# Performance work log

Hardware: AMD Instinct MI355X
Metric: run time of the kernel (lower is better)

Reference implementation:

```python
import jax, jax.numpy as jnp
import numpy as np

B, T, U, D = 2, 512, 48, 512
H, K = 1024, 128  # hidden_channels, num_classes; fc1 in = 2*D = 1024


def setup_inputs() -> dict:
    key = jax.random.key(0)
    ks = jax.random.split(key, 9)
    s = 0.02
    return {
        "img_feature": jax.random.normal(ks[0], (B, T, D), jnp.float32),
        "label_feature": jax.random.normal(ks[1], (B, U, D), jnp.float32),
        "masks": jnp.ones((B, 1, T), jnp.float32),
        "W1": jax.random.normal(ks[2], (H, 2 * D), jnp.float32) * s,
        "b1": jnp.zeros((H,), jnp.float32),
        "W2": jax.random.normal(ks[3], (K, H), jnp.float32) * s,
        "b2": jnp.zeros((K,), jnp.float32),
        "conv_w": jax.random.normal(ks[4], (K, D), jnp.float32) * s,
        "conv_b": jnp.zeros((K,), jnp.float32),
    }


def reference(img_feature, label_feature, masks, W1, b1, W2, b2, conv_w, conv_b):
    # pointwise Conv1d over img features: (B,T,D) -> (B,K,T), masked
    img_seg_score = (jnp.einsum('btd,kd->bkt', img_feature, conv_w)
                     + conv_b[None, :, None]) * masks
    # fc1(cat(label, img)) == label @ Wl^T + img @ Wi^T + b1 (broadcast add),
    # avoiding the O(B*U*T*2D) repeat+cat intermediate.
    d = label_feature.shape[-1]
    Wl, Wi = W1[:, :d], W1[:, d:]
    lab = jnp.einsum('bud,hd->buh', label_feature, Wl)  # (B,U,H)
    img = jnp.einsum('btd,hd->bth', img_feature, Wi)    # (B,T,H)
    h = jnp.tanh(lab[:, :, None, :] + img[:, None, :, :] + b1)  # (B,U,T,H)
    joint = jnp.einsum('buth,kh->butk', h, W2) + b2
    joint_score = jax.nn.log_softmax(joint, axis=-1)
    return (img_seg_score, joint_score)
```

## Files before the change

### kernel.cpp

```cpp
#include <hip/hip_runtime.h>
#include <math.h>

#define BB 2
#define TT 512
#define UU 48
#define DD 512
#define HH 1024
#define KK 128

typedef _Float16 f16x8 __attribute__((ext_vector_type(8)));
typedef __fp16 fp16x2_t __attribute__((ext_vector_type(2)));
typedef float floatx4 __attribute__((ext_vector_type(4)));

__device__ __forceinline__ f16x8 tanh8z(f16x8 z) {
    f16x8 o;
#pragma unroll
    for (int i = 0; i < 8; i += 2) {
        float e0 = __builtin_amdgcn_exp2f((float)z[i]);
        float e1 = __builtin_amdgcn_exp2f((float)z[i + 1]);
        float r0 = __builtin_amdgcn_rcpf(e0 + 1.0f);
        float r1 = __builtin_amdgcn_rcpf(e1 + 1.0f);
        fp16x2_t p = __builtin_amdgcn_cvt_pkrtz(fmaf(-2.0f, r0, 1.0f),
                                                fmaf(-2.0f, r1, 1.0f));
        o[i] = (_Float16)p[0];
        o[i + 1] = (_Float16)p[1];
    }
    return o;
}

__global__ __launch_bounds__(256) void mid_kernel5(
    const float* __restrict__ img, const float* __restrict__ labf,
    const float* __restrict__ W1, const float* __restrict__ W2,
    const float* __restrict__ conv_w,
    const float* __restrict__ b1, const float* __restrict__ conv_b,
    const float* __restrict__ masks,
    _Float16* __restrict__ imgHf, _Float16* __restrict__ labHf,
    _Float16* __restrict__ W2s, float* __restrict__ seg_out) {
    int bid = blockIdx.x, tid = threadIdx.x;
    if (bid >= 624) {
        int base = (bid - 624) * 256 + tid;
#pragma unroll
        for (int i = 0; i < 32; ++i) {
            int o = base + i * 4096;
            int hg = o >> 10, kk2 = (o >> 3) & 127, hl = o & 7;
            W2s[o] = (_Float16)W2[(size_t)kk2 * HH + hg * 8 + hl];
        }
        return;
    }
    __shared__ __align__(16) _Float16 a_s[32][72];
    __shared__ __align__(16) _Float16 w_s[4096];
    const float* Arow;
    const float* Wbase;
    int r0, n0b, wstride, region;
    if (bid < 512) {
        region = 0; Arow = img; Wbase = W1 + 512; wstride = 2 * DD;
        int xcd = bid & 7, j = bid >> 3;
        r0 = (j & 31) * 32; n0b = (xcd * 2 + (j >> 5)) * 64;
    } else if (bid < 560) {
        region = 1; Arow = labf; Wbase = W1; wstride = 2 * DD;
        int i = bid - 512; r0 = (i % 3) * 32; n0b = (i / 3) * 64;
    } else {
        region = 2; Arow = img; Wbase = conv_w; wstride = DD;
        int i = bid - 560; r0 = (i >> 1) * 32; n0b = (i & 1) * 64;
    }
    int lane = tid & 63, wv = tid >> 6;
    int m0 = (wv & 1) * 16, n0w = (wv >> 1) * 32;
    int q = lane >> 4, r = lane & 15;
    int arow = tid >> 3, acol = (tid & 7) * 8;
    int wn = tid >> 2, wk0 = (tid & 3) * 16;
    const float* aptr = &Arow[(size_t)(r0 + arow) * DD + acol];
    const float* wptr = &Wbase[(size_t)(n0b + wn) * wstride + wk0];
    floatx4 acc[2] = {};
    float4 pa0, pa1, pw[4];
    pa0 = *(const float4*)aptr;
    pa1 = *(const float4*)(aptr + 4);
#pragma unroll
    for (int i2 = 0; i2 < 4; ++i2) pw[i2] = *(const float4*)(wptr + i2 * 4);
    for (int c = 0; c < 8; ++c) {
        f16x8 av;
        av[0] = (_Float16)pa0.x; av[1] = (_Float16)pa0.y;
        av[2] = (_Float16)pa0.z; av[3] = (_Float16)pa0.w;
        av[4] = (_Float16)pa1.x; av[5] = (_Float16)pa1.y;
        av[6] = (_Float16)pa1.z; av[7] = (_Float16)pa1.w;
        *(f16x8*)&a_s[arow][acol] = av;
        f16x8 w0, w1;
        w0[0] = (_Float16)pw[0].x; w0[1] = (_Float16)pw[0].y;
        w0[2] = (_Float16)pw[0].z; w0[3] = (_Float16)pw[0].w;
        w0[4] = (_Float16)pw[1].x; w0[5] = (_Float16)pw[1].y;
        w0[6] = (_Float16)pw[1].z; w0[7] = (_Float16)pw[1].w;
        w1[0] = (_Float16)pw[2].x; w1[1] = (_Float16)pw[2].y;
        w1[2] = (_Float16)pw[2].z; w1[3] = (_Float16)pw[2].w;
        w1[4] = (_Float16)pw[3].x; w1[5] = (_Float16)pw[3].y;
        w1[6] = (_Float16)pw[3].z; w1[7] = (_Float16)pw[3].w;
        int kg = wk0 >> 3;
        *(f16x8*)&w_s[((kg + 0) * 64 + wn) * 8] = w0;
        *(f16x8*)&w_s[((kg + 1) * 64 + wn) * 8] = w1;
        __syncthreads();
        if (c < 7) {
            int cb = (c + 1) * 64;
            pa0 = *(const float4*)(aptr + cb);
            pa1 = *(const float4*)(aptr + cb + 4);
#pragma unroll
            for (int i2 = 0; i2 < 4; ++i2)
                pw[i2] = *(const float4*)(wptr + cb + i2 * 4);
        }
#pragma unroll
        for (int kt = 0; kt < 2; ++kt) {
            f16x8 af = *(const f16x8*)&a_s[m0 + r][kt * 32 + q * 8];
#pragma unroll
            for (int nt = 0; nt < 2; ++nt) {
                f16x8 bf = *(const f16x8*)
                    &w_s[((kt * 4 + q) * 64 + n0w + nt * 16 + r) * 8];
                acc[nt] = __builtin_amdgcn_mfma_f32_16x16x32_f16(
                    af, bf, acc[nt], 0, 0, 0);
            }
        }
        __syncthreads();
    }
    const float SC = 2.8853900817779268f;
    if (region == 0) {
#pragma unroll
        for (int nt = 0; nt < 2; ++nt) {
            int n = n0b + n0w + nt * 16 + r;
#pragma unroll
            for (int rr = 0; rr < 4; ++rr)
                imgHf[(size_t)(r0 + m0 + 4 * q + rr) * HH + n] =
                    (_Float16)(acc[nt][rr] * SC);
        }
    } else if (region == 1) {
#pragma unroll
        for (int nt = 0; nt < 2; ++nt) {
            int n = n0b + n0w + nt * 16 + r;
            float bv = b1[n];
#pragma unroll
            for (int rr = 0; rr < 4; ++rr)
                labHf[(size_t)(r0 + m0 + 4 * q + rr) * HH + n] =
                    (_Float16)((acc[nt][rr] + bv) * SC);
        }
    } else {
#pragma unroll
        for (int nt = 0; nt < 2; ++nt) {
            int k = n0b + n0w + nt * 16 + r;
            float bv = conv_b[k];
#pragma unroll
            for (int rr = 0; rr < 4; ++rr) {
                int row = r0 + m0 + 4 * q + rr;
                int b = row >> 9, t = row & 511;
                seg_out[((size_t)b * KK + k) * TT + t] =
                    (acc[nt][rr] + bv) * masks[row];
            }
        }
    }
}

__global__ __launch_bounds__(192, 2) void joint_kernel7(
    const _Float16* __restrict__ imgHf,
    const _Float16* __restrict__ labHf,
    const _Float16* __restrict__ W2s,
    const float* __restrict__ b2,
    float* __restrict__ out) {
    __shared__ __align__(16) _Float16 w_s[2][8192];
    int tid = threadIdx.x, bid = blockIdx.x;
    int lane = tid & 63, wv = tid >> 6;
    int q = lane >> 4, r = lane & 15;
    int g0 = bid * 96 + wv * 32;
    int gr0 = g0 + r, gr1 = g0 + 16 + r;
    int bu0 = gr0 >> 9, t0 = gr0 & 511;
    int bu1 = gr1 >> 9, t1 = gr1 & 511;
    const _Float16* ir0 = imgHf + (size_t)(((bu0 >= UU) ? TT : 0) + t0) * HH;
    const _Float16* ir1 = imgHf + (size_t)(((bu1 >= UU) ? TT : 0) + t1) * HH;
    const _Float16* lr0 = labHf + (size_t)bu0 * HH;
    const _Float16* lr1 = labHf + (size_t)bu1 * HH;
    int c0 = q * 8, c1 = 32 + q * 8;
    floatx4 acc0[8] = {}, acc1[8] = {};
#pragma unroll
    for (int j = 0; j < 5; ++j)
        *(f16x8*)&w_s[0][(tid + j * 192) * 8] =
            *(const f16x8*)&W2s[(tid + j * 192) * 8];
    if (tid < 64)
        *(f16x8*)&w_s[0][(tid + 960) * 8] = *(const f16x8*)&W2s[(tid + 960) * 8];
    f16x8 i0A = *(const f16x8*)&ir0[c0], i0B = *(const f16x8*)&ir0[c1];
    f16x8 i1A = *(const f16x8*)&ir1[c0], i1B = *(const f16x8*)&ir1[c1];
    f16x8 l0A = *(const f16x8*)&lr0[c0], l0B = *(const f16x8*)&lr0[c1];
    f16x8 l1A = *(const f16x8*)&lr1[c0], l1B = *(const f16x8*)&lr1[c1];
    __syncthreads();
    for (int c = 0; c < 16; ++c) {
        _Float16* wb = w_s[c & 1];
        f16x8 ni0A, ni0B, ni1A, ni1B, nl0A, nl0B, nl1A, nl1B;
        f16x8 nw0, nw1, nw2, nw3, nw4, nw5;
        if (c < 15) {
            int cb = (c + 1) * 64;
            ni0A = *(const f16x8*)&ir0[cb + c0];
            ni0B = *(const f16x8*)&ir0[cb + c1];
            ni1A = *(const f16x8*)&ir1[cb + c0];
            ni1B = *(const f16x8*)&ir1[cb + c1];
            nl0A = *(const f16x8*)&lr0[cb + c0];
            nl0B = *(const f16x8*)&lr0[cb + c1];
            nl1A = *(const f16x8*)&lr1[cb + c0];
            nl1B = *(const f16x8*)&lr1[cb + c1];
            const _Float16* wsrc = W2s + (size_t)(c + 1) * 8192;
            nw0 = *(const f16x8*)&wsrc[(tid + 0 * 192) * 8];
            nw1 = *(const f16x8*)&wsrc[(tid + 1 * 192) * 8];
            nw2 = *(const f16x8*)&wsrc[(tid + 2 * 192) * 8];
            nw3 = *(const f16x8*)&wsrc[(tid + 3 * 192) * 8];
            nw4 = *(const f16x8*)&wsrc[(tid + 4 * 192) * 8];
            if (tid < 64) nw5 = *(const f16x8*)&wsrc[(tid + 960) * 8];
        }
        f16x8 a0A = tanh8z(i0A + l0A);
        f16x8 a1A = tanh8z(i1A + l1A);
#pragma unroll
        for (int nt = 0; nt < 8; ++nt) {
            f16x8 bf = *(const f16x8*)&wb[(q * 128 + nt * 16 + r) * 8];
            acc0[nt] = __builtin_amdgcn_mfma_f32_16x16x32_f16(
                a0A, bf, acc0[nt], 0, 0, 0);
            acc1[nt] = __builtin_amdgcn_mfma_f32_16x16x32_f16(
                a1A, bf, acc1[nt], 0, 0, 0);
        }
        f16x8 a0B = tanh8z(i0B + l0B);
        f16x8 a1B = tanh8z(i1B + l1B);
#pragma unroll
        for (int nt = 0; nt < 8; ++nt) {
            f16x8 bf = *(const f16x8*)&wb[((4 + q) * 128 + nt * 16 + r) * 8];
            acc0[nt] = __builtin_amdgcn_mfma_f32_16x16x32_f16(
                a0B, bf, acc0[nt], 0, 0, 0);
            acc1[nt] = __builtin_amdgcn_mfma_f32_16x16x32_f16(
                a1B, bf, acc1[nt], 0, 0, 0);
        }
        if (c < 15) {
            _Float16* wn_ = w_s[(c & 1) ^ 1];
            *(f16x8*)&wn_[(tid + 0 * 192) * 8] = nw0;
            *(f16x8*)&wn_[(tid + 1 * 192) * 8] = nw1;
            *(f16x8*)&wn_[(tid + 2 * 192) * 8] = nw2;
            *(f16x8*)&wn_[(tid + 3 * 192) * 8] = nw3;
            *(f16x8*)&wn_[(tid + 4 * 192) * 8] = nw4;
            if (tid < 64) *(f16x8*)&wn_[(tid + 960) * 8] = nw5;
            i0A = ni0A; i0B = ni0B; i1A = ni1A; i1B = ni1B;
            l0A = nl0A; l0B = nl0B; l1A = nl1A; l1B = nl1B;
        }
        __syncthreads();
    }
    float b2v[8];
#pragma unroll
    for (int nt = 0; nt < 8; ++nt) b2v[nt] = b2[nt * 16 + r];
#pragma unroll
    for (int mt = 0; mt < 2; ++mt) {
        float* obase = out + (size_t)(g0 + mt * 16 + 4 * q) * KK;
#pragma unroll
        for (int rr = 0; rr < 4; ++rr) {
            float v[8];
            float mx = -INFINITY;
#pragma unroll
            for (int nt = 0; nt < 8; ++nt) {
                v[nt] = (mt ? acc1[nt][rr] : acc0[nt][rr]) + b2v[nt];
                mx = fmaxf(mx, v[nt]);
            }
            mx = fmaxf(mx, __shfl_xor(mx, 1, 16));
            mx = fmaxf(mx, __shfl_xor(mx, 2, 16));
            mx = fmaxf(mx, __shfl_xor(mx, 4, 16));
            mx = fmaxf(mx, __shfl_xor(mx, 8, 16));
            float s = 0.f;
#pragma unroll
            for (int nt = 0; nt < 8; ++nt) s += __expf(v[nt] - mx);
            s += __shfl_xor(s, 1, 16);
            s += __shfl_xor(s, 2, 16);
            s += __shfl_xor(s, 4, 16);
            s += __shfl_xor(s, 8, 16);
            float lse = mx + __logf(s);
#pragma unroll
            for (int nt = 0; nt < 8; ++nt)
                obase[(size_t)rr * KK + nt * 16 + r] = v[nt] - lse;
        }
    }
}

extern "C" void kernel_launch(void* const* d_in, const int* in_sizes, int n_in,
                              void* d_out, int out_size, void* d_ws, size_t ws_size,
                              hipStream_t stream) {
    const float* img    = (const float*)d_in[0];
    const float* labf   = (const float*)d_in[1];
    const float* masks  = (const float*)d_in[2];
    const float* W1     = (const float*)d_in[3];
    const float* b1     = (const float*)d_in[4];
    const float* W2     = (const float*)d_in[5];
    const float* b2     = (const float*)d_in[6];
    const float* conv_w = (const float*)d_in[7];
    const float* conv_b = (const float*)d_in[8];
    float* out = (float*)d_out;

    _Float16* base  = (_Float16*)d_ws;
    _Float16* imgHf = base;
    _Float16* labHf = imgHf + 1024 * 1024;
    _Float16* W2s   = labHf + 96 * 1024;

    mid_kernel5<<<640, 256, 0, stream>>>(img, labf, W1, W2, conv_w,
                                         b1, conv_b, masks,
                                         imgHf, labHf, W2s, out);
    joint_kernel7<<<512, 192, 0, stream>>>(imgHf, labHf, W2s, b2,
                                           out + (size_t)BB * KK * TT);
}
```

Before: 125.9 us.

## Replace LDS-staged joint kernel with single-wave blocks reading W2 from global

The joint kernel now runs one 64-thread wave per block, each handling 16 rows instead of three waves handling 96 rows. It drops the shared-memory double buffer for W2 and the per-chunk barriers, loading W2 fragments straight from global memory through cache. The goal is to remove synchronization and LDS traffic and to raise the number of blocks in flight. The cost is more global and L2 traffic for W2, since each wave re-reads it with less reuse per fetch, and there is no longer explicit prefetching of the next chunk.

```diff
diff --git a/kernel.cpp b/kernel.cpp
--- a/kernel.cpp
+++ b/kernel.cpp
@@ -153,123 +153,74 @@
     }
 }
 
-__global__ __launch_bounds__(192, 2) void joint_kernel7(
+__global__ __launch_bounds__(64, 3) void joint_kernel12(
     const _Float16* __restrict__ imgHf,
     const _Float16* __restrict__ labHf,
     const _Float16* __restrict__ W2s,
     const float* __restrict__ b2,
     float* __restrict__ out) {
-    __shared__ __align__(16) _Float16 w_s[2][8192];
-    int tid = threadIdx.x, bid = blockIdx.x;
-    int lane = tid & 63, wv = tid >> 6;
-    int q = lane >> 4, r = lane & 15;
-    int g0 = bid * 96 + wv * 32;
-    int gr0 = g0 + r, gr1 = g0 + 16 + r;
-    int bu0 = gr0 >> 9, t0 = gr0 & 511;
-    int bu1 = gr1 >> 9, t1 = gr1 & 511;
-    const _Float16* ir0 = imgHf + (size_t)(((bu0 >= UU) ? TT : 0) + t0) * HH;
-    const _Float16* ir1 = imgHf + (size_t)(((bu1 >= UU) ? TT : 0) + t1) * HH;
-    const _Float16* lr0 = labHf + (size_t)bu0 * HH;
-    const _Float16* lr1 = labHf + (size_t)bu1 * HH;
-    int c0 = q * 8, c1 = 32 + q * 8;
-    floatx4 acc0[8] = {}, acc1[8] = {};
-#pragma unroll
-    for (int j = 0; j < 5; ++j)
-        *(f16x8*)&w_s[0][(tid + j * 192) * 8] =
-            *(const f16x8*)&W2s[(tid + j * 192) * 8];
-    if (tid < 64)
-        *(f16x8*)&w_s[0][(tid + 960) * 8] = *(const f16x8*)&W2s[(tid + 960) * 8];
-    f16x8 i0A = *(const f16x8*)&ir0[c0], i0B = *(const f16x8*)&ir0[c1];
-    f16x8 i1A = *(const f16x8*)&ir1[c0], i1B = *(const f16x8*)&ir1[c1];
-    f16x8 l0A = *(const f16x8*)&lr0[c0], l0B = *(const f16x8*)&lr0[c1];
-    f16x8 l1A = *(const f16x8*)&lr1[c0], l1B = *(const f16x8*)&lr1[c1];
-    __syncthreads();
+    int lane = threadIdx.x, bid = blockIdx.x;
+    int ql = lane >> 4, r = lane & 15;
+    int g0 = bid * 16;
+    int gr = g0 + r;
+    int bu = gr >> 9;
+    int irow = ((bu >= UU) ? TT : 0) + (gr & 511);
+    const _Float16* ip = imgHf + (size_t)irow * HH + ql * 8;
+    const _Float16* lp = labHf + (size_t)bu * HH + ql * 8;
+    const _Float16* wp = W2s + (size_t)ql * 1024 + r * 8;
+    floatx4 acc[8] = {};
+#pragma unroll 2
     for (int c = 0; c < 16; ++c) {
-        _Float16* wb = w_s[c & 1];
-        f16x8 ni0A, ni0B, ni1A, ni1B, nl0A, nl0B, nl1A, nl1B;
-        f16x8 nw0, nw1, nw2, nw3, nw4, nw5;
-        if (c < 15) {
-            int cb = (c + 1) * 64;
-            ni0A = *(const f16x8*)&ir0[cb + c0];
-            ni0B = *(const f16x8*)&ir0[cb + c1];
-            ni1A = *(const f16x8*)&ir1[cb + c0];
-            ni1B = *(const f16x8*)&ir1[cb + c1];
-            nl0A = *(const f16x8*)&lr0[cb + c0];
-            nl0B = *(const f16x8*)&lr0[cb + c1];
-            nl1A = *(const f16x8*)&lr1[cb + c0];
-            nl1B = *(const f16x8*)&lr1[cb + c1];
-            const _Float16* wsrc = W2s + (size_t)(c + 1) * 8192;
-            nw0 = *(const f16x8*)&wsrc[(tid + 0 * 192) * 8];
-            nw1 = *(const f16x8*)&wsrc[(tid + 1 * 192) * 8];
-            nw2 = *(const f16x8*)&wsrc[(tid + 2 * 192) * 8];
-            nw3 = *(const f16x8*)&wsrc[(tid + 3 * 192) * 8];
-            nw4 = *(const f16x8*)&wsrc[(tid + 4 * 192) * 8];
-            if (tid < 64) nw5 = *(const f16x8*)&wsrc[(tid + 960) * 8];
-        }
-        f16x8 a0A = tanh8z(i0A + l0A);
-        f16x8 a1A = tanh8z(i1A + l1A);
+        const _Float16* ipc = ip + c * 64;
+        const _Float16* lpc = lp + c * 64;
+        const _Float16* wpc = wp + c * 8192;
+        f16x8 iA = *(const f16x8*)ipc;
+        f16x8 iB = *(const f16x8*)(ipc + 32);
+        f16x8 lA = *(const f16x8*)lpc;
+        f16x8 lB = *(const f16x8*)(lpc + 32);
+        f16x8 aA = tanh8z(iA + lA);
+        f16x8 aB = tanh8z(iB + lB);
 #pragma unroll
         for (int nt = 0; nt < 8; ++nt) {
-            f16x8 bf = *(const f16x8*)&wb[(q * 128 + nt * 16 + r) * 8];
-            acc0[nt] = __builtin_amdgcn_mfma_f32_16x16x32_f16(
-                a0A, bf, acc0[nt], 0, 0, 0);
-            acc1[nt] = __builtin_amdgcn_mfma_f32_16x16x32_f16(
-                a1A, bf, acc1[nt], 0, 0, 0);
-        }
-        f16x8 a0B = tanh8z(i0B + l0B);
-        f16x8 a1B = tanh8z(i1B + l1B);
+            f16x8 bf = *(const f16x8*)(wpc + nt * 128);
+            acc[nt] = __builtin_amdgcn_mfma_f32_16x16x32_f16(
+                aA, bf, acc[nt], 0, 0, 0);
+        }
 #pragma unroll
         for (int nt = 0; nt < 8; ++nt) {
-            f16x8 bf = *(const f16x8*)&wb[((4 + q) * 128 + nt * 16 + r) * 8];
-            acc0[nt] = __builtin_amdgcn_mfma_f32_16x16x32_f16(
-                a0B, bf, acc0[nt], 0, 0, 0);
-            acc1[nt] = __builtin_amdgcn_mfma_f32_16x16x32_f16(
-                a1B, bf, acc1[nt], 0, 0, 0);
-        }
-        if (c < 15) {
-            _Float16* wn_ = w_s[(c & 1) ^ 1];
-            *(f16x8*)&wn_[(tid + 0 * 192) * 8] = nw0;
-            *(f16x8*)&wn_[(tid + 1 * 192) * 8] = nw1;
-            *(f16x8*)&wn_[(tid + 2 * 192) * 8] = nw2;
-            *(f16x8*)&wn_[(tid + 3 * 192) * 8] = nw3;
-            *(f16x8*)&wn_[(tid + 4 * 192) * 8] = nw4;
-            if (tid < 64) *(f16x8*)&wn_[(tid + 960) * 8] = nw5;
-            i0A = ni0A; i0B = ni0B; i1A = ni1A; i1B = ni1B;
-            l0A = nl0A; l0B = nl0B; l1A = nl1A; l1B = nl1B;
-        }
-        __syncthreads();
+            f16x8 bf = *(const f16x8*)(wpc + 4096 + nt * 128);
+            acc[nt] = __builtin_amdgcn_mfma_f32_16x16x32_f16(
+                aB, bf, acc[nt], 0, 0, 0);
+        }
     }
     float b2v[8];
 #pragma unroll
     for (int nt = 0; nt < 8; ++nt) b2v[nt] = b2[nt * 16 + r];
 #pragma unroll
-    for (int mt = 0; mt < 2; ++mt) {
-        float* obase = out + (size_t)(g0 + mt * 16 + 4 * q) * KK;
-#pragma unroll
-        for (int rr = 0; rr < 4; ++rr) {
-            float v[8];
-            float mx = -INFINITY;
-#pragma unroll
-            for (int nt = 0; nt < 8; ++nt) {
-                v[nt] = (mt ? acc1[nt][rr] : acc0[nt][rr]) + b2v[nt];
-                mx = fmaxf(mx, v[nt]);
-            }
-            mx = fmaxf(mx, __shfl_xor(mx, 1, 16));
-            mx = fmaxf(mx, __shfl_xor(mx, 2, 16));
-            mx = fmaxf(mx, __shfl_xor(mx, 4, 16));
-            mx = fmaxf(mx, __shfl_xor(mx, 8, 16));
-            float s = 0.f;
-#pragma unroll
-            for (int nt = 0; nt < 8; ++nt) s += __expf(v[nt] - mx);
-            s += __shfl_xor(s, 1, 16);
-            s += __shfl_xor(s, 2, 16);
-            s += __shfl_xor(s, 4, 16);
-            s += __shfl_xor(s, 8, 16);
-            float lse = mx + __logf(s);
-#pragma unroll
-            for (int nt = 0; nt < 8; ++nt)
-                obase[(size_t)rr * KK + nt * 16 + r] = v[nt] - lse;
-        }
+    for (int rr = 0; rr < 4; ++rr) {
+        float v[8];
+        float mx = -INFINITY;
+#pragma unroll
+        for (int nt = 0; nt < 8; ++nt) {
+            v[nt] = acc[nt][rr] + b2v[nt];
+            mx = fmaxf(mx, v[nt]);
+        }
+        mx = fmaxf(mx, __shfl_xor(mx, 1, 16));
+        mx = fmaxf(mx, __shfl_xor(mx, 2, 16));
+        mx = fmaxf(mx, __shfl_xor(mx, 4, 16));
+        mx = fmaxf(mx, __shfl_xor(mx, 8, 16));
+        float s = 0.f;
+#pragma unroll
+        for (int nt = 0; nt < 8; ++nt) s += __expf(v[nt] - mx);
+        s += __shfl_xor(s, 1, 16);
+        s += __shfl_xor(s, 2, 16);
+        s += __shfl_xor(s, 4, 16);
+        s += __shfl_xor(s, 8, 16);
+        float lse = mx + __logf(s);
+        float* orow = out + (size_t)(g0 + 4 * ql + rr) * KK;
+#pragma unroll
+        for (int nt = 0; nt < 8; ++nt)
+            orow[nt * 16 + r] = v[nt] - lse;
     }
 }
 
@@ -295,6 +246,6 @@
     mid_kernel5<<<640, 256, 0, stream>>>(img, labf, W1, W2, conv_w,
                                          b1, conv_b, masks,
                                          imgHf, labHf, W2s, out);
-    joint_kernel7<<<512, 192, 0, stream>>>(imgHf, labHf, W2s, b2,
-                                           out + (size_t)BB * KK * TT);
-}
+    joint_kernel12<<<3072, 64, 0, stream>>>(imgHf, labHf, W2s, b2,
+                                            out + (size_t)BB * KK * TT);
+}
```

New measurement: 162.0 us. 1.29x slower.
